# Optimization experiments

Measured on AMD Instinct MI355X. Metric: run time of the kernel, lower is better.

The kernel has to match this reference:

```python
import jax, jax.numpy as jnp
import numpy as np

HIDDEN = 150

def setup_inputs() -> dict:
    key = jax.random.key(0)
    ks = jax.random.split(key, 6)
    B, N, E = 1, 512, 256
    G = 3 * E  # gij_dim = 768
    embeds = jax.random.normal(ks[0], (B, N, E), dtype=jnp.float32)
    mention_scores = jax.random.normal(ks[1], (B, N, 1), dtype=jnp.float32)
    W1 = jax.random.normal(ks[2], (G, HIDDEN), dtype=jnp.float32) * (1.0 / np.sqrt(G))
    b1 = jnp.zeros((HIDDEN,), dtype=jnp.float32)
    W2 = jax.random.normal(ks[3], (HIDDEN, HIDDEN), dtype=jnp.float32) * (1.0 / np.sqrt(HIDDEN))
    b2 = jnp.zeros((HIDDEN,), dtype=jnp.float32)
    W3 = jax.random.normal(ks[4], (HIDDEN, 1), dtype=jnp.float32) * (1.0 / np.sqrt(HIDDEN))
    b3 = jnp.zeros((1,), dtype=jnp.float32)
    return {"batch_document_span_embeds": embeds, "mention_scores": mention_scores,
            "W1": W1, "b1": b1, "W2": W2, "b2": b2, "W3": W3, "b3": b3}


def reference(batch_document_span_embeds, mention_scores, W1, b1, W2, b2, W3, b3):
    g = batch_document_span_embeds            # [B, N, E]
    gi = g[:, :, None, :]                     # span_1 broadcast -> [B, N, 1, E]
    gj = g[:, None, :, :]                     # span_2 broadcast -> [B, 1, N, E]
    B, N, E = g.shape
    # pairwise feature cat((s1, s2, s1*s2)) -> [B, N, N, 3E]
    pair = jnp.concatenate([
        jnp.broadcast_to(gi, (B, N, N, E)),
        jnp.broadcast_to(gj, (B, N, N, E)),
        gi * gj,
    ], axis=-1)
    # small MLP score (dropout is inference-mode identity)
    h = jax.nn.relu(pair @ W1 + b1)           # [B, N, N, 150]
    h = jax.nn.relu(h @ W2 + b2)              # [B, N, N, 150]
    s = h @ W3 + b3                           # [B, N, N, 1]
    # mean of (mention_i, mention_j, pair_ij)
    out = (mention_scores[:, :, None, :] + mention_scores[:, None, :, :] + s) / 3.0
    return out                                # [B, N, N, 1]
```

## Files before the change

### kernel.cpp

```cpp
#include <hip/hip_runtime.h>

#define N  512
#define E  256
#define H  150
#define HP 160
#define JB 64
#define NCH (N / JB)

typedef __attribute__((ext_vector_type(8))) short short8;
typedef __attribute__((ext_vector_type(4))) float f32x4;
typedef __attribute__((ext_vector_type(4))) unsigned uint4v;
typedef __attribute__((ext_vector_type(2))) unsigned uint2v;

__device__ __forceinline__ unsigned short f2bf(float f) {
    unsigned u = __float_as_uint(f);
    u += 0x7fffu + ((u >> 16) & 1u);
    return (unsigned short)(u >> 16);
}
__device__ __forceinline__ unsigned pkbf(float a, float b) {
    return (unsigned)f2bf(a) | ((unsigned)f2bf(b) << 16);
}

__global__ __launch_bounds__(192) void precompute_ab(
    const float* __restrict__ g, const float* __restrict__ W1,
    const float* __restrict__ b1, float* __restrict__ wsA,
    unsigned short* __restrict__ wsB)
{
    const int i0  = blockIdx.x * 4;
    const int tid = threadIdx.x;
    __shared__ float gi[4][E];
    for (int idx = tid; idx < 4 * E; idx += 192) gi[idx >> 8][idx & 255] = g[i0 * E + idx];
    __syncthreads();
    const int h = tid;
    if (h < HP) {
        float a[4] = {0, 0, 0, 0}, b[4] = {0, 0, 0, 0};
        if (h < H) {
            for (int e = 0; e < E; ++e) {
                const float wa = W1[e * H + h];
                const float wb = W1[(E + e) * H + h];
#pragma unroll
                for (int qq = 0; qq < 4; ++qq) {
                    a[qq] = fmaf(gi[qq][e], wa, a[qq]);
                    b[qq] = fmaf(gi[qq][e], wb, b[qq]);
                }
            }
            const float bb = b1[h];
#pragma unroll
            for (int qq = 0; qq < 4; ++qq) a[qq] += bb;
        }
#pragma unroll
        for (int qq = 0; qq < 4; ++qq) {
            wsA[(i0 + qq) * HP + h] = a[qq];
            wsB[(i0 + qq) * HP + h] = f2bf(b[qq]);
        }
    }
}

#define OFF_P   0
#define OFF_H1  33792
#define OFF_C2  55296
#define OFF_W3L 55936
#define OFF_SB  56576
#define LDS_SZ  57600

__global__ __launch_bounds__(512, 2) void pairwise_mfma(
    const float* __restrict__ g,  const float* __restrict__ ms,
    const float* __restrict__ W1, const float* __restrict__ W2,
    const float* __restrict__ b2, const float* __restrict__ W3,
    const float* __restrict__ b3, const float* __restrict__ wsA,
    const unsigned short* __restrict__ wsB, float* __restrict__ out)
{
    __shared__ __attribute__((aligned(16))) char smem[LDS_SZ];
    float* smf = (float*)smem;
    const int tid  = threadIdx.x;
    const int wave = tid >> 6;
    const int lane = tid & 63;
    const int c    = lane & 15;
    const int q    = lane >> 4;
    const int wq   = wave & 3;
    const int jh   = wave >> 2;
    const int hbase  = (wq < 2) ? wq * 48 : 96 + (wq - 2) * 32;
    const int mcount = (wq < 2) ? 3 : 2;
    const short8 z8 = {0, 0, 0, 0, 0, 0, 0, 0};

    short8 w1f[3][8];
    for (int p = 0; p < 2; ++p) {
        if (p) __syncthreads();
        if (tid < 300) {
            const int h = (tid < 150) ? tid : tid - 150;
            const int half = (tid < 150) ? 0 : 1;
            const float* wsrc = W1 + (2 * E + p * 128) * H + h;
            char* dst = smem + h * 272 + half * 128;
#pragma unroll 4
            for (int t = 0; t < 32; ++t) {
                const int ep = half * 32 + t;
                *(unsigned*)(dst + t * 4) = pkbf(wsrc[(2 * ep) * H], wsrc[(2 * ep + 1) * H]);
            }
        }
        __syncthreads();
#pragma unroll
        for (int m = 0; m < 3; ++m) {
            const int hr = hbase + m * 16 + c;
#pragma unroll
            for (int ktp = 0; ktp < 4; ++ktp)
                w1f[m][p * 4 + ktp] = (m < mcount && hr < H)
                    ? *(const short8*)(smem + hr * 272 + (ktp * 32 + q * 8) * 2) : z8;
        }
    }
    __syncthreads();
    if (tid < 300) {
        const int h = (tid < 150) ? tid : tid - 150;
        const int half = (tid < 150) ? 0 : 1;
        char* dst = smem + h * 336;
#pragma unroll 4
        for (int t = 0; t < 42; ++t) {
            const int kp = half * 42 + t;
            const float lo = (2 * kp     < H) ? W2[(2 * kp) * H + h]     : 0.0f;
            const float hi = (2 * kp + 1 < H) ? W2[(2 * kp + 1) * H + h] : 0.0f;
            *(unsigned*)(dst + kp * 4) = pkbf(lo, hi);
        }
    }
    if (tid >= 320 && tid < 480) {
        const int hx = tid - 320;
        smf[OFF_C2 / 4 + hx]  = (hx < H) ? b2[hx] : 0.0f;
        smf[OFF_W3L / 4 + hx] = (hx < H) ? W3[hx] : 0.0f;
    }
    __syncthreads();
    short8 w2f[3][5];
#pragma unroll
    for (int m = 0; m < 3; ++m) {
        const int hr = hbase + m * 16 + c;
#pragma unroll
        for (int kt = 0; kt < 5; ++kt)
            w2f[m][kt] = (m < mcount && hr < H)
                ? *(const short8*)(smem + hr * 336 + (kt * 32 + q * 8) * 2) : z8;
    }
    __syncthreads();

    const int jb = tid >> 5;
    const int e0 = (tid & 31) * 8;
    const float b3v = b3[0];
    const int i = blockIdx.x;
    const f32x4 ga = *(const f32x4*)(g + i * E + e0);
    const f32x4 gb = *(const f32x4*)(g + i * E + e0 + 4);
    f32x4 av[3];
#pragma unroll
    for (int m = 0; m < 3; ++m)
        av[m] = (m < mcount) ? *(const f32x4*)(wsA + i * HP + hbase + m * 16 + q * 4)
                             : (f32x4){0, 0, 0, 0};
    const float msi = ms[i];

#pragma unroll
    for (int it = 0; it < 4; ++it) {
        const int jl = jb + it * 16;
        const float* gr = g + jl * E + e0;
        const f32x4 u = *(const f32x4*)gr;
        const f32x4 v = *(const f32x4*)(gr + 4);
        uint4v pk;
        pk[0] = pkbf(u[0] * ga[0], u[1] * ga[1]);
        pk[1] = pkbf(u[2] * ga[2], u[3] * ga[3]);
        pk[2] = pkbf(v[0] * gb[0], v[1] * gb[1]);
        pk[3] = pkbf(v[2] * gb[2], v[3] * gb[3]);
        *(uint4v*)(smem + OFF_P + jl * 528 + e0 * 2) = pk;
    }
    __syncthreads();

    for (int ch = 0; ch < NCH; ++ch) {
        const int j0 = ch * JB;

        f32x4 acc[2][3];
#pragma unroll
        for (int jt = 0; jt < 2; ++jt)
#pragma unroll
            for (int m = 0; m < 3; ++m) acc[jt][m] = (f32x4){0, 0, 0, 0};
#pragma unroll
        for (int kt = 0; kt < 8; ++kt) {
            short8 pf[2];
#pragma unroll
            for (int jt = 0; jt < 2; ++jt)
                pf[jt] = *(const short8*)(smem + OFF_P + (jh * 32 + jt * 16 + c) * 528 + (kt * 32 + q * 8) * 2);
#pragma unroll
            for (int m = 0; m < 3; ++m)
                if (m < mcount)
#pragma unroll
                    for (int jt = 0; jt < 2; ++jt)
                        acc[jt][m] = __builtin_amdgcn_mfma_f32_16x16x32_bf16(w1f[m][kt], pf[jt], acc[jt][m], 0, 0, 0);
        }
#pragma unroll
        for (int m = 0; m < 3; ++m)
            if (m < mcount) {
                const int h0 = hbase + m * 16 + q * 4;
#pragma unroll
                for (int jt = 0; jt < 2; ++jt) {
                    const int j = jh * 32 + jt * 16 + c;
                    const uint2v bv = *(const uint2v*)(wsB + (j0 + j) * HP + h0);
                    const float v0 = fmaxf(acc[jt][m][0] + av[m][0] + __uint_as_float(bv[0] << 16), 0.0f);
                    const float v1 = fmaxf(acc[jt][m][1] + av[m][1] + __uint_as_float(bv[0] & 0xffff0000u), 0.0f);
                    const float v2 = fmaxf(acc[jt][m][2] + av[m][2] + __uint_as_float(bv[1] << 16), 0.0f);
                    const float v3 = fmaxf(acc[jt][m][3] + av[m][3] + __uint_as_float(bv[1] & 0xffff0000u), 0.0f);
                    uint2v hw;
                    hw[0] = pkbf(v0, v1);
                    hw[1] = pkbf(v2, v3);
                    *(uint2v*)(smem + OFF_H1 + j * 336 + h0 * 2) = hw;
                }
            }
        __syncthreads();

#pragma unroll
        for (int jt = 0; jt < 2; ++jt)
#pragma unroll
            for (int m = 0; m < 3; ++m) acc[jt][m] = (f32x4){0, 0, 0, 0};
#pragma unroll
        for (int kt = 0; kt < 5; ++kt) {
            short8 hf[2];
#pragma unroll
            for (int jt = 0; jt < 2; ++jt)
                hf[jt] = *(const short8*)(smem + OFF_H1 + (jh * 32 + jt * 16 + c) * 336 + (kt * 32 + q * 8) * 2);
#pragma unroll
            for (int m = 0; m < 3; ++m)
                if (m < mcount)
#pragma unroll
                    for (int jt = 0; jt < 2; ++jt)
                        acc[jt][m] = __builtin_amdgcn_mfma_f32_16x16x32_bf16(w2f[m][kt], hf[jt], acc[jt][m], 0, 0, 0);
        }
        float part[2] = {0.0f, 0.0f};
#pragma unroll
        for (int m = 0; m < 3; ++m)
            if (m < mcount) {
                const int h0 = hbase + m * 16 + q * 4;
                const f32x4 b2v = *(const f32x4*)(smf + OFF_C2 / 4 + h0);
                const f32x4 w3v = *(const f32x4*)(smf + OFF_W3L / 4 + h0);
#pragma unroll
                for (int jt = 0; jt < 2; ++jt)
#pragma unroll
                    for (int r = 0; r < 4; ++r)
                        part[jt] = fmaf(fmaxf(acc[jt][m][r] + b2v[r], 0.0f), w3v[r], part[jt]);
            }
#pragma unroll
        for (int jt = 0; jt < 2; ++jt) {
            float pv = part[jt];
            pv += __shfl_xor(pv, 16);
            pv += __shfl_xor(pv, 32);
            if (q == 0) smf[OFF_SB / 4 + wq * 64 + jh * 32 + jt * 16 + c] = pv;
        }
        if (ch + 1 < NCH) {
            const int jn = (ch + 1) * JB;
#pragma unroll
            for (int it = 0; it < 4; ++it) {
                const int jl = jb + it * 16;
                const float* gr = g + (jn + jl) * E + e0;
                const f32x4 u = *(const f32x4*)gr;
                const f32x4 v = *(const f32x4*)(gr + 4);
                uint4v pk;
                pk[0] = pkbf(u[0] * ga[0], u[1] * ga[1]);
                pk[1] = pkbf(u[2] * ga[2], u[3] * ga[3]);
                pk[2] = pkbf(v[0] * gb[0], v[1] * gb[1]);
                pk[3] = pkbf(v[2] * gb[2], v[3] * gb[3]);
                *(uint4v*)(smem + OFF_P + jl * 528 + e0 * 2) = pk;
            }
        }
        __syncthreads();

        if (tid < JB) {
            const int j = j0 + tid;
            const float s = smf[OFF_SB / 4 + tid] + smf[OFF_SB / 4 + 64 + tid]
                          + smf[OFF_SB / 4 + 128 + tid] + smf[OFF_SB / 4 + 192 + tid] + b3v;
            out[i * N + j] = (msi + ms[j] + s) * (1.0f / 3.0f);
        }
    }
}

extern "C" void kernel_launch(void* const* d_in, const int* in_sizes, int n_in,
                              void* d_out, int out_size, void* d_ws, size_t ws_size,
                              hipStream_t stream) {
    const float* g  = (const float*)d_in[0];
    const float* ms = (const float*)d_in[1];
    const float* W1 = (const float*)d_in[2];
    const float* b1 = (const float*)d_in[3];
    const float* W2 = (const float*)d_in[4];
    const float* b2 = (const float*)d_in[5];
    const float* W3 = (const float*)d_in[6];
    const float* b3 = (const float*)d_in[7];
    float* out = (float*)d_out;
    float* wsA = (float*)d_ws;
    unsigned short* wsB = (unsigned short*)((char*)d_ws + N * HP * 4);

    precompute_ab<<<N / 4, 192, 0, stream>>>(g, W1, b1, wsA, wsB);
    pairwise_mfma<<<N, 512, 0, stream>>>(g, ms, W1, W2, b2, W3, b3, wsA, wsB, out);
}
```

Before: 177.0 us.

## Process two query rows per block to amortize weight staging

Each block of the pairwise kernel now handles two consecutive rows i instead of one, and the grid is halved. The per-block prologue, which converts W1 and W2 to bf16 in LDS and loads them into register fragments, is therefore paid once per two rows. The prologue's LDS writes are also widened from 4-byte to 16-byte stores. The trade-off is fewer blocks, which may reduce latency hiding and load balance across CUs, and a longer serial loop in each block.

Result: faster. 171.8 us (-2.9%).

```diff
diff --git a/kernel.cpp b/kernel.cpp
--- a/kernel.cpp
+++ b/kernel.cpp
@@ -87,14 +87,19 @@
     for (int p = 0; p < 2; ++p) {
         if (p) __syncthreads();
         if (tid < 300) {
-            const int h = (tid < 150) ? tid : tid - 150;
+            const int h    = (tid < 150) ? tid : tid - 150;
             const int half = (tid < 150) ? 0 : 1;
             const float* wsrc = W1 + (2 * E + p * 128) * H + h;
             char* dst = smem + h * 272 + half * 128;
-#pragma unroll 4
-            for (int t = 0; t < 32; ++t) {
-                const int ep = half * 32 + t;
-                *(unsigned*)(dst + t * 4) = pkbf(wsrc[(2 * ep) * H], wsrc[(2 * ep + 1) * H]);
+#pragma unroll
+            for (int t = 0; t < 8; ++t) {
+                const int e8 = (half * 8 + t) * 8;
+                uint4v pk;
+                pk[0] = pkbf(wsrc[(e8 + 0) * H], wsrc[(e8 + 1) * H]);
+                pk[1] = pkbf(wsrc[(e8 + 2) * H], wsrc[(e8 + 3) * H]);
+                pk[2] = pkbf(wsrc[(e8 + 4) * H], wsrc[(e8 + 5) * H]);
+                pk[3] = pkbf(wsrc[(e8 + 6) * H], wsrc[(e8 + 7) * H]);
+                *(uint4v*)(dst + t * 16) = pk;
             }
         }
         __syncthreads();
@@ -109,15 +114,21 @@
     }
     __syncthreads();
     if (tid < 300) {
-        const int h = (tid < 150) ? tid : tid - 150;
-        const int half = (tid < 150) ? 0 : 1;
+        const int h  = (tid < 150) ? tid : tid - 150;
+        const int lo = (tid < 150) ? 0 : 11;
+        const int hi = (tid < 150) ? 11 : 21;
         char* dst = smem + h * 336;
-#pragma unroll 4
-        for (int t = 0; t < 42; ++t) {
-            const int kp = half * 42 + t;
-            const float lo = (2 * kp     < H) ? W2[(2 * kp) * H + h]     : 0.0f;
-            const float hi = (2 * kp + 1 < H) ? W2[(2 * kp + 1) * H + h] : 0.0f;
-            *(unsigned*)(dst + kp * 4) = pkbf(lo, hi);
+        for (int t = lo; t < hi; ++t) {
+            const int k8 = t * 8;
+            uint4v pk;
+#pragma unroll
+            for (int x = 0; x < 4; ++x) {
+                const int ka = k8 + 2 * x, kb = k8 + 2 * x + 1;
+                const float va = (ka < H) ? W2[ka * H + h] : 0.0f;
+                const float vb = (kb < H) ? W2[kb * H + h] : 0.0f;
+                pk[x] = pkbf(va, vb);
+            }
+            *(uint4v*)(dst + t * 16) = pk;
         }
     }
     if (tid >= 320 && tid < 480) {
@@ -140,132 +151,135 @@
     const int jb = tid >> 5;
     const int e0 = (tid & 31) * 8;
     const float b3v = b3[0];
-    const int i = blockIdx.x;
-    const f32x4 ga = *(const f32x4*)(g + i * E + e0);
-    const f32x4 gb = *(const f32x4*)(g + i * E + e0 + 4);
-    f32x4 av[3];
-#pragma unroll
-    for (int m = 0; m < 3; ++m)
-        av[m] = (m < mcount) ? *(const f32x4*)(wsA + i * HP + hbase + m * 16 + q * 4)
-                             : (f32x4){0, 0, 0, 0};
-    const float msi = ms[i];
-
-#pragma unroll
-    for (int it = 0; it < 4; ++it) {
-        const int jl = jb + it * 16;
-        const float* gr = g + jl * E + e0;
-        const f32x4 u = *(const f32x4*)gr;
-        const f32x4 v = *(const f32x4*)(gr + 4);
-        uint4v pk;
-        pk[0] = pkbf(u[0] * ga[0], u[1] * ga[1]);
-        pk[1] = pkbf(u[2] * ga[2], u[3] * ga[3]);
-        pk[2] = pkbf(v[0] * gb[0], v[1] * gb[1]);
-        pk[3] = pkbf(v[2] * gb[2], v[3] * gb[3]);
-        *(uint4v*)(smem + OFF_P + jl * 528 + e0 * 2) = pk;
-    }
-    __syncthreads();
-
-    for (int ch = 0; ch < NCH; ++ch) {
-        const int j0 = ch * JB;
-
-        f32x4 acc[2][3];
-#pragma unroll
-        for (int jt = 0; jt < 2; ++jt)
-#pragma unroll
-            for (int m = 0; m < 3; ++m) acc[jt][m] = (f32x4){0, 0, 0, 0};
-#pragma unroll
-        for (int kt = 0; kt < 8; ++kt) {
-            short8 pf[2];
+
+    for (int ii = 0; ii < 2; ++ii) {
+        const int i = blockIdx.x * 2 + ii;
+        const f32x4 ga = *(const f32x4*)(g + i * E + e0);
+        const f32x4 gb = *(const f32x4*)(g + i * E + e0 + 4);
+        f32x4 av[3];
+#pragma unroll
+        for (int m = 0; m < 3; ++m)
+            av[m] = (m < mcount) ? *(const f32x4*)(wsA + i * HP + hbase + m * 16 + q * 4)
+                                 : (f32x4){0, 0, 0, 0};
+        const float msi = ms[i];
+
+#pragma unroll
+        for (int it = 0; it < 4; ++it) {
+            const int jl = jb + it * 16;
+            const float* gr = g + jl * E + e0;
+            const f32x4 u = *(const f32x4*)gr;
+            const f32x4 v = *(const f32x4*)(gr + 4);
+            uint4v pk;
+            pk[0] = pkbf(u[0] * ga[0], u[1] * ga[1]);
+            pk[1] = pkbf(u[2] * ga[2], u[3] * ga[3]);
+            pk[2] = pkbf(v[0] * gb[0], v[1] * gb[1]);
+            pk[3] = pkbf(v[2] * gb[2], v[3] * gb[3]);
+            *(uint4v*)(smem + OFF_P + jl * 528 + e0 * 2) = pk;
+        }
+        __syncthreads();
+
+        for (int ch = 0; ch < NCH; ++ch) {
+            const int j0 = ch * JB;
+
+            f32x4 acc[2][3];
 #pragma unroll
             for (int jt = 0; jt < 2; ++jt)
-                pf[jt] = *(const short8*)(smem + OFF_P + (jh * 32 + jt * 16 + c) * 528 + (kt * 32 + q * 8) * 2);
+#pragma unroll
+                for (int m = 0; m < 3; ++m) acc[jt][m] = (f32x4){0, 0, 0, 0};
+#pragma unroll
+            for (int kt = 0; kt < 8; ++kt) {
+                short8 pf[2];
+#pragma unroll
+                for (int jt = 0; jt < 2; ++jt)
+                    pf[jt] = *(const short8*)(smem + OFF_P + (jh * 32 + jt * 16 + c) * 528 + (kt * 32 + q * 8) * 2);
+#pragma unroll
+                for (int m = 0; m < 3; ++m)
+                    if (m < mcount)
+#pragma unroll
+                        for (int jt = 0; jt < 2; ++jt)
+                            acc[jt][m] = __builtin_amdgcn_mfma_f32_16x16x32_bf16(w1f[m][kt], pf[jt], acc[jt][m], 0, 0, 0);
+            }
 #pragma unroll
             for (int m = 0; m < 3; ++m)
-                if (m < mcount)
+                if (m < mcount) {
+                    const int h0 = hbase + m * 16 + q * 4;
+#pragma unroll
+                    for (int jt = 0; jt < 2; ++jt) {
+                        const int j = jh * 32 + jt * 16 + c;
+                        const uint2v bv = *(const uint2v*)(wsB + (j0 + j) * HP + h0);
+                        const float v0 = fmaxf(acc[jt][m][0] + av[m][0] + __uint_as_float(bv[0] << 16), 0.0f);
+                        const float v1 = fmaxf(acc[jt][m][1] + av[m][1] + __uint_as_float(bv[0] & 0xffff0000u), 0.0f);
+                        const float v2 = fmaxf(acc[jt][m][2] + av[m][2] + __uint_as_float(bv[1] << 16), 0.0f);
+                        const float v3 = fmaxf(acc[jt][m][3] + av[m][3] + __uint_as_float(bv[1] & 0xffff0000u), 0.0f);
+                        uint2v hw;
+                        hw[0] = pkbf(v0, v1);
+                        hw[1] = pkbf(v2, v3);
+                        *(uint2v*)(smem + OFF_H1 + j * 336 + h0 * 2) = hw;
+                    }
+                }
+            __syncthreads();
+
+#pragma unroll
+            for (int jt = 0; jt < 2; ++jt)
+#pragma unroll
+                for (int m = 0; m < 3; ++m) acc[jt][m] = (f32x4){0, 0, 0, 0};
+#pragma unroll
+            for (int kt = 0; kt < 5; ++kt) {
+                short8 hf[2];
+#pragma unroll
+                for (int jt = 0; jt < 2; ++jt)
+                    hf[jt] = *(const short8*)(smem + OFF_H1 + (jh * 32 + jt * 16 + c) * 336 + (kt * 32 + q * 8) * 2);
+#pragma unroll
+                for (int m = 0; m < 3; ++m)
+                    if (m < mcount)
+#pragma unroll
+                        for (int jt = 0; jt < 2; ++jt)
+                            acc[jt][m] = __builtin_amdgcn_mfma_f32_16x16x32_bf16(w2f[m][kt], hf[jt], acc[jt][m], 0, 0, 0);
+            }
+            float part[2] = {0.0f, 0.0f};
+#pragma unroll
+            for (int m = 0; m < 3; ++m)
+                if (m < mcount) {
+                    const int h0 = hbase + m * 16 + q * 4;
+                    const f32x4 b2v = *(const f32x4*)(smf + OFF_C2 / 4 + h0);
+                    const f32x4 w3v = *(const f32x4*)(smf + OFF_W3L / 4 + h0);
 #pragma unroll
                     for (int jt = 0; jt < 2; ++jt)
-                        acc[jt][m] = __builtin_amdgcn_mfma_f32_16x16x32_bf16(w1f[m][kt], pf[jt], acc[jt][m], 0, 0, 0);
-        }
-#pragma unroll
-        for (int m = 0; m < 3; ++m)
-            if (m < mcount) {
-                const int h0 = hbase + m * 16 + q * 4;
-#pragma unroll
-                for (int jt = 0; jt < 2; ++jt) {
-                    const int j = jh * 32 + jt * 16 + c;
-                    const uint2v bv = *(const uint2v*)(wsB + (j0 + j) * HP + h0);
-                    const float v0 = fmaxf(acc[jt][m][0] + av[m][0] + __uint_as_float(bv[0] << 16), 0.0f);
-                    const float v1 = fmaxf(acc[jt][m][1] + av[m][1] + __uint_as_float(bv[0] & 0xffff0000u), 0.0f);
-                    const float v2 = fmaxf(acc[jt][m][2] + av[m][2] + __uint_as_float(bv[1] << 16), 0.0f);
-                    const float v3 = fmaxf(acc[jt][m][3] + av[m][3] + __uint_as_float(bv[1] & 0xffff0000u), 0.0f);
-                    uint2v hw;
-                    hw[0] = pkbf(v0, v1);
-                    hw[1] = pkbf(v2, v3);
-                    *(uint2v*)(smem + OFF_H1 + j * 336 + h0 * 2) = hw;
+#pragma unroll
+                        for (int r = 0; r < 4; ++r)
+                            part[jt] = fmaf(fmaxf(acc[jt][m][r] + b2v[r], 0.0f), w3v[r], part[jt]);
                 }
-            }
-        __syncthreads();
-
-#pragma unroll
-        for (int jt = 0; jt < 2; ++jt)
-#pragma unroll
-            for (int m = 0; m < 3; ++m) acc[jt][m] = (f32x4){0, 0, 0, 0};
-#pragma unroll
-        for (int kt = 0; kt < 5; ++kt) {
-            short8 hf[2];
-#pragma unroll
-            for (int jt = 0; jt < 2; ++jt)
-                hf[jt] = *(const short8*)(smem + OFF_H1 + (jh * 32 + jt * 16 + c) * 336 + (kt * 32 + q * 8) * 2);
-#pragma unroll
-            for (int m = 0; m < 3; ++m)
-                if (m < mcount)
-#pragma unroll
-                    for (int jt = 0; jt < 2; ++jt)
-                        acc[jt][m] = __builtin_amdgcn_mfma_f32_16x16x32_bf16(w2f[m][kt], hf[jt], acc[jt][m], 0, 0, 0);
-        }
-        float part[2] = {0.0f, 0.0f};
-#pragma unroll
-        for (int m = 0; m < 3; ++m)
-            if (m < mcount) {
-                const int h0 = hbase + m * 16 + q * 4;
-                const f32x4 b2v = *(const f32x4*)(smf + OFF_C2 / 4 + h0);
-                const f32x4 w3v = *(const f32x4*)(smf + OFF_W3L / 4 + h0);
-#pragma unroll
-                for (int jt = 0; jt < 2; ++jt)
-#pragma unroll
-                    for (int r = 0; r < 4; ++r)
-                        part[jt] = fmaf(fmaxf(acc[jt][m][r] + b2v[r], 0.0f), w3v[r], part[jt]);
-            }
-#pragma unroll
-        for (int jt = 0; jt < 2; ++jt) {
-            float pv = part[jt];
-            pv += __shfl_xor(pv, 16);
-            pv += __shfl_xor(pv, 32);
-            if (q == 0) smf[OFF_SB / 4 + wq * 64 + jh * 32 + jt * 16 + c] = pv;
-        }
-        if (ch + 1 < NCH) {
-            const int jn = (ch + 1) * JB;
-#pragma unroll
-            for (int it = 0; it < 4; ++it) {
-                const int jl = jb + it * 16;
-                const float* gr = g + (jn + jl) * E + e0;
-                const f32x4 u = *(const f32x4*)gr;
-                const f32x4 v = *(const f32x4*)(gr + 4);
-                uint4v pk;
-                pk[0] = pkbf(u[0] * ga[0], u[1] * ga[1]);
-                pk[1] = pkbf(u[2] * ga[2], u[3] * ga[3]);
-                pk[2] = pkbf(v[0] * gb[0], v[1] * gb[1]);
-                pk[3] = pkbf(v[2] * gb[2], v[3] * gb[3]);
-                *(uint4v*)(smem + OFF_P + jl * 528 + e0 * 2) = pk;
-            }
-        }
-        __syncthreads();
-
-        if (tid < JB) {
-            const int j = j0 + tid;
-            const float s = smf[OFF_SB / 4 + tid] + smf[OFF_SB / 4 + 64 + tid]
-                          + smf[OFF_SB / 4 + 128 + tid] + smf[OFF_SB / 4 + 192 + tid] + b3v;
-            out[i * N + j] = (msi + ms[j] + s) * (1.0f / 3.0f);
+#pragma unroll
+            for (int jt = 0; jt < 2; ++jt) {
+                float pv = part[jt];
+                pv += __shfl_xor(pv, 16);
+                pv += __shfl_xor(pv, 32);
+                if (q == 0) smf[OFF_SB / 4 + wq * 64 + jh * 32 + jt * 16 + c] = pv;
+            }
+            if (ch + 1 < NCH) {
+                const int jn = (ch + 1) * JB;
+#pragma unroll
+                for (int it = 0; it < 4; ++it) {
+                    const int jl = jb + it * 16;
+                    const float* gr = g + (jn + jl) * E + e0;
+                    const f32x4 u = *(const f32x4*)gr;
+                    const f32x4 v = *(const f32x4*)(gr + 4);
+                    uint4v pk;
+                    pk[0] = pkbf(u[0] * ga[0], u[1] * ga[1]);
+                    pk[1] = pkbf(u[2] * ga[2], u[3] * ga[3]);
+                    pk[2] = pkbf(v[0] * gb[0], v[1] * gb[1]);
+                    pk[3] = pkbf(v[2] * gb[2], v[3] * gb[3]);
+                    *(uint4v*)(smem + OFF_P + jl * 528 + e0 * 2) = pk;
+                }
+            }
+            __syncthreads();
+
+            if (tid < JB) {
+                const int j = j0 + tid;
+                const float s = smf[OFF_SB / 4 + tid] + smf[OFF_SB / 4 + 64 + tid]
+                              + smf[OFF_SB / 4 + 128 + tid] + smf[OFF_SB / 4 + 192 + tid] + b3v;
+                out[i * N + j] = (msi + ms[j] + s) * (1.0f / 3.0f);
+            }
         }
     }
 }
@@ -286,5 +300,5 @@
     unsigned short* wsB = (unsigned short*)((char*)d_ws + N * HP * 4);
 
     precompute_ab<<<N / 4, 192, 0, stream>>>(g, W1, b1, wsA, wsB);
-    pairwise_mfma<<<N, 512, 0, stream>>>(g, ms, W1, W2, b2, W3, b3, wsA, wsB, out);
-}
+    pairwise_mfma<<<N / 2, 512, 0, stream>>>(g, ms, W1, W2, b2, W3, b3, wsA, wsB, out);
+}
```
